# Kernel tuning notes

Hardware: AMD Instinct MI355X
Metric: run time of the kernel (lower is better)

## Reference

```python
import jax, jax.numpy as jnp
import numpy as np

N = 50000      # nodes (single node type 'mapping_var')
IN = 128       # in_feats
HID = 128      # hid_feats
OUT = 64       # out_feats
R = 3          # number of relations
E = 800000     # edges per relation (avg degree 16)
NEG_SLOPE = 0.01  # F.leaky_relu default


def setup_inputs() -> dict:
    key = jax.random.key(0)
    ks = jax.random.split(key, 9)
    s = 0.05
    return {
        "x": jax.random.normal(ks[0], (N, IN), jnp.float32),
        "edge_src": jax.random.randint(ks[1], (R, E), 0, N, jnp.int32),
        "edge_dst": jax.random.randint(ks[2], (R, E), 0, N, jnp.int32),
        "W0": jax.random.normal(ks[3], (R, IN, HID), jnp.float32) * s,
        "b0": jnp.zeros((R, HID), jnp.float32),
        "Wl": jax.random.normal(ks[4], (4, R, HID, HID), jnp.float32) * s,
        "bl": jnp.zeros((4, R, HID), jnp.float32),
        "Wout": jax.random.normal(ks[5], (HID, OUT), jnp.float32) * s,
        "bout": jnp.zeros((OUT,), jnp.float32),
    }


def _hetero_conv(h, edge_src, edge_dst, W, b):
    """One HeteroGraphConv layer: per-relation GraphConv (norm='both') then
    mean-aggregate across relations.  h: [N, Din], W: [R, Din, Dout]."""
    ones = jnp.ones((E,), h.dtype)
    outs = []
    for r in range(R):
        src, dst = edge_src[r], edge_dst[r]
        out_deg = jax.ops.segment_sum(ones, src, num_segments=N)
        in_deg = jax.ops.segment_sum(ones, dst, num_segments=N)
        # src-side normalization D_out^{-1/2}
        hn = h * jax.lax.rsqrt(jnp.maximum(out_deg, 1.0))[:, None]
        # gather messages along edges, sum into destinations
        agg = jax.ops.segment_sum(hn[src], dst, num_segments=N)
        # dst-side normalization D_in^{-1/2}
        agg = agg * jax.lax.rsqrt(jnp.maximum(in_deg, 1.0))[:, None]
        outs.append(agg @ W[r] + b[r])
    return jnp.mean(jnp.stack(outs, axis=0), axis=0)  # 'mean' cross-relation aggregate


def reference(x, edge_src, edge_dst, W0, b0, Wl, bl, Wout, bout):
    # Layer 0: in_feats -> hid_feats
    h = _hetero_conv(x, edge_src, edge_dst, W0, b0)
    h = jax.nn.leaky_relu(h, NEG_SLOPE)  # dropout omitted (eval mode)
    # Layers 1..4: hid -> hid; activation after all but the last
    for l in range(4):
        h = _hetero_conv(h, edge_src, edge_dst, Wl[l], bl[l])
        if l != 3:
            h = jax.nn.leaky_relu(h, NEG_SLOPE)
    # final Linear on h['mapping_var']
    return h @ Wout + bout
```

## Files before the change

kernel.cpp:

```cpp
#include <hip/hip_runtime.h>
#include <hip/hip_bf16.h>
#include <cstddef>
#include <cstdint>

#define NNODES 50000
#define NR 3
#define NE 800000
#define HIDF 128
#define OUTF 64
#define NEG_SLOPE 0.01f
#define SCAN_T 1024
#define NCHUNK ((NNODES + SCAN_T - 1) / SCAN_T)
#define KTOT (NR * HIDF)
#define KU (KTOT / 2)

__device__ __forceinline__ float bf_lo(uint v) { return __uint_as_float(v << 16); }
__device__ __forceinline__ float bf_hi(uint v) { return __uint_as_float(v & 0xffff0000u); }
__device__ __forceinline__ uint bf_rne(float f) {
    uint u = __float_as_uint(f);
    return (u + 0x7fffu + ((u >> 16) & 1u)) >> 16;
}
__device__ __forceinline__ uint bf_pack(float a, float b) {
    return bf_rne(a) | (bf_rne(b) << 16);
}

typedef short bf16x8 __attribute__((ext_vector_type(8)));
typedef float f32x4 __attribute__((ext_vector_type(4)));
__device__ __forceinline__ bf16x8 as_bf(uint4 v) { return __builtin_bit_cast(bf16x8, v); }

__global__ __launch_bounds__(256) void k_cast_x(const float* __restrict__ x,
                                                uint* __restrict__ xb) {
    int i = blockIdx.x * blockDim.x + threadIdx.x;
    if (i >= NNODES * (HIDF / 2)) return;
    float2 v = *(const float2*)(x + (size_t)i * 2);
    xb[i] = bf_pack(v.x, v.y);
}

__global__ __launch_bounds__(256) void k_cast_w(const float* __restrict__ W0,
                                                const float* __restrict__ Wl,
                                                uint* __restrict__ wbT) {
    int idx = blockIdx.x * blockDim.x + threadIdx.x;
    if (idx >= 5 * HIDF * KU) return;
    int l = idx / (HIDF * KU);
    int rem = idx - l * (HIDF * KU);
    int t = rem / HIDF;
    int n = rem - t * HIDF;
    int r = t / 64;
    int kk = (t - r * 64) * 2;
    const float* Wsrc = (l == 0) ? W0 : Wl + (size_t)(l - 1) * NR * HIDF * HIDF;
    const float* wp = Wsrc + ((size_t)r * HIDF + kk) * HIDF + n;
    float a = wp[0];
    float b = wp[HIDF];
    wbT[(size_t)l * HIDF * KU + (size_t)n * KU + t] = bf_pack(a, b);
}

__global__ __launch_bounds__(256) void k_count(const int* __restrict__ esrc,
                                               const int* __restrict__ edst,
                                               int* __restrict__ deg_out,
                                               int* __restrict__ deg_in,
                                               ushort* __restrict__ epos) {
    int idx = blockIdx.x * blockDim.x + threadIdx.x;
    if (idx >= NR * NE) return;
    int r = idx / NE;
    int s = esrc[idx];
    int d = edst[idx];
    atomicAdd(&deg_out[r * NNODES + s], 1);
    int p = atomicAdd(&deg_in[r * NNODES + d], 1);
    epos[idx] = (ushort)p;
}

__global__ __launch_bounds__(256) void k_norms(const int* __restrict__ deg_out,
                                               const int* __restrict__ deg_in,
                                               float* __restrict__ out_norm,
                                               float* __restrict__ in_norm) {
    int idx = blockIdx.x * blockDim.x + threadIdx.x;
    if (idx >= NR * NNODES) return;
    int dout = deg_out[idx];
    int din  = deg_in[idx];
    out_norm[idx] = rsqrtf((float)(dout > 1 ? dout : 1));
    in_norm[idx]  = rsqrtf((float)(din  > 1 ? din  : 1));
}

__global__ __launch_bounds__(SCAN_T) void k_scan1(const int* __restrict__ deg_in,
                                                  int* __restrict__ row_ptr,
                                                  int* __restrict__ csums) {
    __shared__ int buf[SCAN_T];
    int r = blockIdx.x / NCHUNK;
    int c = blockIdx.x % NCHUNK;
    int tid = threadIdx.x;
    int i = c * SCAN_T + tid;
    int v = (i < NNODES) ? deg_in[r * NNODES + i] : 0;
    buf[tid] = v;
    __syncthreads();
    for (int off = 1; off < SCAN_T; off <<= 1) {
        int t = (tid >= off) ? buf[tid - off] : 0;
        __syncthreads();
        buf[tid] += t;
        __syncthreads();
    }
    if (i < NNODES) row_ptr[r * (NNODES + 1) + i + 1] = buf[tid];
    if (tid == SCAN_T - 1) csums[r * NCHUNK + c] = buf[SCAN_T - 1];
}

__global__ void k_scan2(const int* __restrict__ csums, int* __restrict__ coffs) {
    int r = threadIdx.x;
    if (r >= NR) return;
    int run = 0;
    for (int c = 0; c < NCHUNK; ++c) {
        coffs[r * NCHUNK + c] = run;
        run += csums[r * NCHUNK + c];
    }
}

__global__ __launch_bounds__(SCAN_T) void k_scan3(int* __restrict__ row_ptr,
                                                  const int* __restrict__ coffs) {
    int r = blockIdx.x / NCHUNK;
    int c = blockIdx.x % NCHUNK;
    int tid = threadIdx.x;
    int i = c * SCAN_T + tid;
    int off = coffs[r * NCHUNK + c];
    if (i < NNODES) row_ptr[r * (NNODES + 1) + i + 1] += off;
    if (tid == 0 && c == 0) row_ptr[r * (NNODES + 1)] = 0;
}

__global__ __launch_bounds__(256) void k_fill_csr(const int* __restrict__ esrc,
                                                  const int* __restrict__ edst,
                                                  const int* __restrict__ row_ptr,
                                                  const ushort* __restrict__ epos,
                                                  const float* __restrict__ out_norm,
                                                  int2* __restrict__ csr_sw) {
    int idx = blockIdx.x * blockDim.x + threadIdx.x;
    if (idx >= NR * NE) return;
    int r = idx / NE;
    int s = esrc[idx];
    int d = edst[idx];
    float w = out_norm[r * NNODES + s];
    int slot = row_ptr[r * (NNODES + 1) + d] + (int)epos[idx];
    csr_sw[(size_t)r * NE + slot] = make_int2(s, __float_as_int(w));
}

__global__ __launch_bounds__(256) void k_aggregate(const uint* __restrict__ hin,
                                                   const float* __restrict__ in_norm,
                                                   const int* __restrict__ row_ptr,
                                                   const int2* __restrict__ csr_sw,
                                                   uint* __restrict__ aggb) {
    int wave = blockIdx.x * 4 + (threadIdx.x >> 6);
    if (wave >= NR * NNODES) return;
    int r = wave / NNODES;
    int n = wave - r * NNODES;
    int lane = threadIdx.x & 63;
    int start = row_ptr[r * (NNODES + 1) + n];
    int end   = row_ptr[r * (NNODES + 1) + n + 1];
    const int2* cw = csr_sw + (size_t)r * NE;
    float acc0 = 0.f, acc1 = 0.f;
    int i = start;
    for (; i + 8 <= end; i += 8) {
        int2 e[8];
        uint v[8];
#pragma unroll
        for (int j = 0; j < 8; ++j) e[j] = cw[i + j];
#pragma unroll
        for (int j = 0; j < 8; ++j) v[j] = hin[(size_t)e[j].x * (HIDF / 2) + lane];
#pragma unroll
        for (int j = 0; j < 8; ++j) {
            float w = __int_as_float(e[j].y);
            acc0 = fmaf(w, bf_lo(v[j]), acc0);
            acc1 = fmaf(w, bf_hi(v[j]), acc1);
        }
    }
    for (; i + 4 <= end; i += 4) {
        int2 e[4];
        uint v[4];
#pragma unroll
        for (int j = 0; j < 4; ++j) e[j] = cw[i + j];
#pragma unroll
        for (int j = 0; j < 4; ++j) v[j] = hin[(size_t)e[j].x * (HIDF / 2) + lane];
#pragma unroll
        for (int j = 0; j < 4; ++j) {
            float w = __int_as_float(e[j].y);
            acc0 = fmaf(w, bf_lo(v[j]), acc0);
            acc1 = fmaf(w, bf_hi(v[j]), acc1);
        }
    }
    for (; i < end; ++i) {
        int2 e = cw[i];
        float w = __int_as_float(e.y);
        uint v = hin[(size_t)e.x * (HIDF / 2) + lane];
        acc0 = fmaf(w, bf_lo(v), acc0);
        acc1 = fmaf(w, bf_hi(v), acc1);
    }
    float wn = in_norm[r * NNODES + n];
    aggb[(size_t)n * KU + r * (HIDF / 2) + lane] = bf_pack(acc0 * wn, acc1 * wn);
}

__global__ __launch_bounds__(256) void k_conv_mm(const uint* __restrict__ aggb,
                                                 const uint* __restrict__ wbT,
                                                 const float* __restrict__ bias,
                                                 ushort* __restrict__ hout,
                                                 int act) {
    int wv   = threadIdx.x >> 6;
    int lane = threadIdx.x & 63;
    int lrow = lane & 15;
    int kgrp = lane >> 4;
    int rb = blockIdx.x * 128 + wv * 32;

    f32x4 acc[2][8];
#pragma unroll
    for (int m = 0; m < 2; ++m)
#pragma unroll
        for (int nr = 0; nr < 8; ++nr) acc[m][nr] = (f32x4){0.f, 0.f, 0.f, 0.f};

    int row0 = rb + lrow;
    int row1 = rb + 16 + lrow;
    bool v0 = row0 < NNODES;
    bool v1 = row1 < NNODES;
    const uint* a0p = aggb + (size_t)row0 * KU + kgrp * 4;
    const uint* a1p = aggb + (size_t)row1 * KU + kgrp * 4;
    const uint* bp  = wbT + (size_t)lrow * KU + kgrp * 4;
    const uint4 za = make_uint4(0u, 0u, 0u, 0u);

#pragma unroll
    for (int ks = 0; ks < KTOT / 32; ++ks) {
        uint4 ua0 = v0 ? *(const uint4*)(a0p + ks * 16) : za;
        uint4 ua1 = v1 ? *(const uint4*)(a1p + ks * 16) : za;
        bf16x8 af0 = as_bf(ua0);
        bf16x8 af1 = as_bf(ua1);
#pragma unroll
        for (int nr = 0; nr < 8; ++nr) {
            uint4 ub = *(const uint4*)(bp + (size_t)nr * (16 * KU) + ks * 16);
            bf16x8 bf = as_bf(ub);
            acc[0][nr] = __builtin_amdgcn_mfma_f32_16x16x32_bf16(af0, bf, acc[0][nr], 0, 0, 0);
            acc[1][nr] = __builtin_amdgcn_mfma_f32_16x16x32_bf16(af1, bf, acc[1][nr], 0, 0, 0);
        }
    }

    const float inv3 = 1.f / 3.f;
#pragma unroll
    for (int nr = 0; nr < 8; ++nr) {
        int col = nr * 16 + lrow;
        float bm = (bias[col] + bias[HIDF + col] + bias[2 * HIDF + col]) * inv3;
#pragma unroll
        for (int m = 0; m < 2; ++m) {
            int rbase = rb + m * 16 + kgrp * 4;
#pragma unroll
            for (int i = 0; i < 4; ++i) {
                int row = rbase + i;
                if (row >= NNODES) continue;
                float t = acc[m][nr][i] * inv3 + bm;
                if (act) t = (t > 0.f) ? t : NEG_SLOPE * t;
                hout[(size_t)row * HIDF + col] = (ushort)bf_rne(t);
            }
        }
    }
}

__global__ __launch_bounds__(256) void k_final(const uint* __restrict__ h,
                                               const float* __restrict__ Wout,
                                               const float* __restrict__ bout,
                                               float* __restrict__ out) {
    int tid = threadIdx.x;
    int col = tid & 63;
    int row = blockIdx.x * 4 + (tid >> 6);
    if (row >= NNODES) return;
    const uint* hp = h + (size_t)row * (HIDF / 2);
    float acc = bout[col];
#pragma unroll 8
    for (int ku = 0; ku < HIDF / 2; ++ku) {
        uint v = hp[ku];
        acc = fmaf(bf_lo(v), Wout[(2 * ku) * OUTF + col], acc);
        acc = fmaf(bf_hi(v), Wout[(2 * ku + 1) * OUTF + col], acc);
    }
    out[(size_t)row * OUTF + col] = acc;
}

extern "C" void kernel_launch(void* const* d_in, const int* in_sizes, int n_in,
                              void* d_out, int out_size, void* d_ws, size_t ws_size,
                              hipStream_t stream) {
    const float* x    = (const float*)d_in[0];
    const int*   esrc = (const int*)d_in[1];
    const int*   edst = (const int*)d_in[2];
    const float* W0   = (const float*)d_in[3];
    const float* b0   = (const float*)d_in[4];
    const float* Wl   = (const float*)d_in[5];
    const float* bl   = (const float*)d_in[6];
    const float* Wout = (const float*)d_in[7];
    const float* bout = (const float*)d_in[8];
    float* out = (float*)d_out;

    char* ws = (char*)d_ws;
    size_t off = 0;
    auto carve = [&](size_t bytes) {
        size_t p = off;
        off += (bytes + 255) & ~(size_t)255;
        return p;
    };
    const size_t SZ_RN_I = (size_t)NR * NNODES * 4;
    size_t o_deg_out = carve(SZ_RN_I);
    size_t o_deg_in  = carve(SZ_RN_I);
    size_t zero_span = off;
    size_t o_out_nrm = carve(SZ_RN_I);
    size_t o_in_nrm  = carve(SZ_RN_I);
    size_t o_row_ptr = carve((size_t)NR * (NNODES + 1) * 4);
    size_t o_csums   = carve((size_t)NR * NCHUNK * 4);
    size_t o_coffs   = carve((size_t)NR * NCHUNK * 4);
    size_t o_csr     = carve((size_t)NR * NE * 8);
    size_t o_epos    = carve((size_t)NR * NE * 2);
    size_t o_aggb    = carve((size_t)NNODES * KU * 4);
    size_t o_xb      = carve((size_t)NNODES * (HIDF / 2) * 4);
    size_t o_h       = carve((size_t)NNODES * (HIDF / 2) * 4);
    size_t o_wbT     = carve((size_t)5 * HIDF * KU * 4);
    (void)ws_size;

    int*    deg_out  = (int*)(ws + o_deg_out);
    int*    deg_in   = (int*)(ws + o_deg_in);
    float*  out_norm = (float*)(ws + o_out_nrm);
    float*  in_norm  = (float*)(ws + o_in_nrm);
    int*    row_ptr  = (int*)(ws + o_row_ptr);
    int*    csums    = (int*)(ws + o_csums);
    int*    coffs    = (int*)(ws + o_coffs);
    int2*   csr_sw   = (int2*)(ws + o_csr);
    ushort* epos     = (ushort*)(ws + o_epos);
    uint*   aggb     = (uint*)(ws + o_aggb);
    uint*   xb       = (uint*)(ws + o_xb);
    uint*   h        = (uint*)(ws + o_h);
    uint*   wbT      = (uint*)(ws + o_wbT);

    hipMemsetAsync(ws, 0, zero_span, stream);

    int nEdgeBlocks = (NR * NE + 255) / 256;
    k_cast_x<<<(NNODES * (HIDF / 2) + 255) / 256, 256, 0, stream>>>(x, xb);
    k_cast_w<<<(5 * HIDF * KU + 255) / 256, 256, 0, stream>>>(W0, Wl, wbT);
    k_count<<<nEdgeBlocks, 256, 0, stream>>>(esrc, edst, deg_out, deg_in, epos);
    k_norms<<<(NR * NNODES + 255) / 256, 256, 0, stream>>>(deg_out, deg_in, out_norm, in_norm);
    k_scan1<<<NR * NCHUNK, SCAN_T, 0, stream>>>(deg_in, row_ptr, csums);
    k_scan2<<<1, 64, 0, stream>>>(csums, coffs);
    k_scan3<<<NR * NCHUNK, SCAN_T, 0, stream>>>(row_ptr, coffs);
    k_fill_csr<<<nEdgeBlocks, 256, 0, stream>>>(esrc, edst, row_ptr, epos, out_norm, csr_sw);

    const int aggBlocks = (NR * NNODES + 3) / 4;
    const int mmBlocks  = (NNODES + 127) / 128;

    const uint* hin = xb;
    for (int l = 0; l < 5; ++l) {
        k_aggregate<<<aggBlocks, 256, 0, stream>>>(hin, in_norm, row_ptr, csr_sw, aggb);
        const uint*  Wp = wbT + (size_t)l * HIDF * KU;
        const float* bp = (l == 0) ? b0 : bl + (size_t)(l - 1) * NR * HIDF;
        k_conv_mm<<<mmBlocks, 256, 0, stream>>>(aggb, Wp, bp, (ushort*)h, (l < 4) ? 1 : 0);
        hin = h;
    }
    k_final<<<(NNODES + 3) / 4, 256, 0, stream>>>(h, Wout, bout, out);
}
```

Measured before the change: 1.119 ms.

## Privatize degree-count atomics per XCD to avoid cross-die atomic traffic

Degree counting now uses one private counter array per XCD, updated with workgroup-scope relaxed atomics that can stay in the local L2. A merge kernel sums the eight copies into the degrees and norms and builds per-XCD prefix offsets, which the CSR fill uses to compute each edge's slot. This targets the cost of device-scope atomics that bounce between dies. In exchange it adds eight times the counter memory to zero and read, plus an extra prefix array. Correctness depends on each XCD's L2 being coherent for workgroup-scope atomics, and on per-XCD in-degree counts fitting in 12 bits.

```diff
diff --git a/kernel.cpp b/kernel.cpp
--- a/kernel.cpp
+++ b/kernel.cpp
@@ -13,6 +13,8 @@
 #define NCHUNK ((NNODES + SCAN_T - 1) / SCAN_T)
 #define KTOT (NR * HIDF)
 #define KU (KTOT / 2)
+#define RN (NR * NNODES)
+#define NXCD 8
 
 __device__ __forceinline__ float bf_lo(uint v) { return __uint_as_float(v << 16); }
 __device__ __forceinline__ float bf_hi(uint v) { return __uint_as_float(v & 0xffff0000u); }
@@ -27,6 +29,12 @@
 typedef short bf16x8 __attribute__((ext_vector_type(8)));
 typedef float f32x4 __attribute__((ext_vector_type(4)));
 __device__ __forceinline__ bf16x8 as_bf(uint4 v) { return __builtin_bit_cast(bf16x8, v); }
+
+__device__ __forceinline__ int xcc_id() {
+    int x;
+    asm volatile("s_getreg_b32 %0, hwreg(HW_REG_XCC_ID)" : "=s"(x));
+    return x & (NXCD - 1);
+}
 
 __global__ __launch_bounds__(256) void k_cast_x(const float* __restrict__ x,
                                                 uint* __restrict__ xb) {
@@ -56,29 +64,42 @@
 
 __global__ __launch_bounds__(256) void k_count(const int* __restrict__ esrc,
                                                const int* __restrict__ edst,
-                                               int* __restrict__ deg_out,
-                                               int* __restrict__ deg_in,
+                                               int* __restrict__ dego8,
+                                               int* __restrict__ degi8,
                                                ushort* __restrict__ epos) {
     int idx = blockIdx.x * blockDim.x + threadIdx.x;
     if (idx >= NR * NE) return;
+    int xcd = xcc_id();
     int r = idx / NE;
     int s = esrc[idx];
     int d = edst[idx];
-    atomicAdd(&deg_out[r * NNODES + s], 1);
-    int p = atomicAdd(&deg_in[r * NNODES + d], 1);
-    epos[idx] = (ushort)p;
-}
-
-__global__ __launch_bounds__(256) void k_norms(const int* __restrict__ deg_out,
-                                               const int* __restrict__ deg_in,
+    __hip_atomic_fetch_add(&dego8[(size_t)xcd * RN + r * NNODES + s], 1,
+                           __ATOMIC_RELAXED, __HIP_MEMORY_SCOPE_WORKGROUP);
+    int p = __hip_atomic_fetch_add(&degi8[(size_t)xcd * RN + r * NNODES + d], 1,
+                                   __ATOMIC_RELAXED, __HIP_MEMORY_SCOPE_WORKGROUP);
+    epos[idx] = (ushort)((p & 0xfff) | (xcd << 12));
+}
+
+__global__ __launch_bounds__(256) void k_merge(const int* __restrict__ dego8,
+                                               const int* __restrict__ degi8,
+                                               int* __restrict__ deg_in,
+                                               int* __restrict__ xpref,
                                                float* __restrict__ out_norm,
                                                float* __restrict__ in_norm) {
     int idx = blockIdx.x * blockDim.x + threadIdx.x;
-    if (idx >= NR * NNODES) return;
-    int dout = deg_out[idx];
-    int din  = deg_in[idx];
-    out_norm[idx] = rsqrtf((float)(dout > 1 ? dout : 1));
-    in_norm[idx]  = rsqrtf((float)(din  > 1 ? din  : 1));
+    if (idx >= RN) return;
+    int so = 0;
+#pragma unroll
+    for (int x = 0; x < NXCD; ++x) so += dego8[(size_t)x * RN + idx];
+    int si = 0;
+#pragma unroll
+    for (int x = 0; x < NXCD; ++x) {
+        xpref[(size_t)x * RN + idx] = si;
+        si += degi8[(size_t)x * RN + idx];
+    }
+    deg_in[idx] = si;
+    out_norm[idx] = rsqrtf((float)(so > 1 ? so : 1));
+    in_norm[idx]  = rsqrtf((float)(si > 1 ? si : 1));
 }
 
 __global__ __launch_bounds__(SCAN_T) void k_scan1(const int* __restrict__ deg_in,
@@ -127,6 +148,7 @@
                                                   const int* __restrict__ edst,
                                                   const int* __restrict__ row_ptr,
                                                   const ushort* __restrict__ epos,
+                                                  const int* __restrict__ xpref,
                                                   const float* __restrict__ out_norm,
                                                   int2* __restrict__ csr_sw) {
     int idx = blockIdx.x * blockDim.x + threadIdx.x;
@@ -135,7 +157,10 @@
     int s = esrc[idx];
     int d = edst[idx];
     float w = out_norm[r * NNODES + s];
-    int slot = row_ptr[r * (NNODES + 1) + d] + (int)epos[idx];
+    ushort e = epos[idx];
+    int slot = row_ptr[r * (NNODES + 1) + d]
+             + xpref[(size_t)(e >> 12) * RN + r * NNODES + d]
+             + (e & 0xfff);
     csr_sw[(size_t)r * NE + slot] = make_int2(s, __float_as_int(w));
 }
 
@@ -294,10 +319,12 @@
         off += (bytes + 255) & ~(size_t)255;
         return p;
     };
-    const size_t SZ_RN_I = (size_t)NR * NNODES * 4;
-    size_t o_deg_out = carve(SZ_RN_I);
+    const size_t SZ_RN_I = (size_t)RN * 4;
+    size_t o_dego8   = carve((size_t)NXCD * RN * 4);
+    size_t o_degi8   = carve((size_t)NXCD * RN * 4);
+    size_t zero_span = off;
     size_t o_deg_in  = carve(SZ_RN_I);
-    size_t zero_span = off;
+    size_t o_xpref   = carve((size_t)NXCD * RN * 4);
     size_t o_out_nrm = carve(SZ_RN_I);
     size_t o_in_nrm  = carve(SZ_RN_I);
     size_t o_row_ptr = carve((size_t)NR * (NNODES + 1) * 4);
@@ -311,8 +338,10 @@
     size_t o_wbT     = carve((size_t)5 * HIDF * KU * 4);
     (void)ws_size;
 
-    int*    deg_out  = (int*)(ws + o_deg_out);
+    int*    dego8    = (int*)(ws + o_dego8);
+    int*    degi8    = (int*)(ws + o_degi8);
     int*    deg_in   = (int*)(ws + o_deg_in);
+    int*    xpref    = (int*)(ws + o_xpref);
     float*  out_norm = (float*)(ws + o_out_nrm);
     float*  in_norm  = (float*)(ws + o_in_nrm);
     int*    row_ptr  = (int*)(ws + o_row_ptr);
@@ -330,12 +359,12 @@
     int nEdgeBlocks = (NR * NE + 255) / 256;
     k_cast_x<<<(NNODES * (HIDF / 2) + 255) / 256, 256, 0, stream>>>(x, xb);
     k_cast_w<<<(5 * HIDF * KU + 255) / 256, 256, 0, stream>>>(W0, Wl, wbT);
-    k_count<<<nEdgeBlocks, 256, 0, stream>>>(esrc, edst, deg_out, deg_in, epos);
-    k_norms<<<(NR * NNODES + 255) / 256, 256, 0, stream>>>(deg_out, deg_in, out_norm, in_norm);
+    k_count<<<nEdgeBlocks, 256, 0, stream>>>(esrc, edst, dego8, degi8, epos);
+    k_merge<<<(RN + 255) / 256, 256, 0, stream>>>(dego8, degi8, deg_in, xpref, out_norm, in_norm);
     k_scan1<<<NR * NCHUNK, SCAN_T, 0, stream>>>(deg_in, row_ptr, csums);
     k_scan2<<<1, 64, 0, stream>>>(csums, coffs);
     k_scan3<<<NR * NCHUNK, SCAN_T, 0, stream>>>(row_ptr, coffs);
-    k_fill_csr<<<nEdgeBlocks, 256, 0, stream>>>(esrc, edst, row_ptr, epos, out_norm, csr_sw);
+    k_fill_csr<<<nEdgeBlocks, 256, 0, stream>>>(esrc, edst, row_ptr, epos, xpref, out_norm, csr_sw);
 
     const int aggBlocks = (NR * NNODES + 3) / 4;
     const int mmBlocks  = (NNODES + 127) / 128;
```

Result: no change. 1.129 ms (+0.9%).
